# Optimization experiments

Hardware: AMD Instinct MI355X
Metric: run time of the kernel (lower is better)

Reference implementation:

```python
import jax, jax.numpy as jnp
import numpy as np

N_NODES = 50000
N_EDGES = 800000
D = 128
H = 8
DH = D // H  # 16


def setup_inputs() -> dict:
    key = jax.random.key(0)
    ks = jax.random.split(key, 9)
    x = jax.random.normal(ks[0], (N_NODES, D), dtype=jnp.float32)
    # guarantee every node has >=1 incoming edge (avoids z == 0)
    dst_rand = jax.random.randint(ks[1], (N_EDGES - N_NODES,), 0, N_NODES, dtype=jnp.int64 if jax.config.jax_enable_x64 else jnp.int32)
    dst = jnp.concatenate([jnp.arange(N_NODES, dtype=dst_rand.dtype), dst_rand])
    src = jax.random.randint(ks[2], (N_EDGES,), 0, N_NODES, dtype=dst.dtype)
    scale = 0.05
    Wq = jax.random.normal(ks[3], (D, D), dtype=jnp.float32) * scale
    Wk = jax.random.normal(ks[4], (D, D), dtype=jnp.float32) * scale
    Wv = jax.random.normal(ks[5], (D, D), dtype=jnp.float32) * scale
    bq = jax.random.normal(ks[6], (D,), dtype=jnp.float32) * scale
    bk = jax.random.normal(ks[7], (D,), dtype=jnp.float32) * scale
    bv = jax.random.normal(ks[8], (D,), dtype=jnp.float32) * scale
    return {"x": x, "src": src, "dst": dst, "Wq": Wq, "bq": bq, "Wk": Wk, "bk": bk, "Wv": Wv, "bv": bv}


def reference(x, src, dst, Wq, bq, Wk, bk, Wv, bv):
    N = x.shape[0]
    # node projections -> [N, H, DH]
    Q = (x @ Wq + bq).reshape(N, H, DH)
    K = (x @ Wk + bk).reshape(N, H, DH)
    V = (x @ Wv + bv).reshape(N, H, DH)
    scale_const = jnp.sqrt(jnp.float32(DH))
    # per-edge score: (K[src] . Q[dst]) per head, then exp-clamp  -> [E, H]
    score = jnp.einsum('ehd,ehd->eh', K[src], Q[dst])
    score = jnp.exp(jnp.clip(score / scale_const, -5.0, 5.0))
    # scatter-sum by destination node
    wV = jax.ops.segment_sum(score[:, :, None] * V[src], dst, num_segments=N)  # [N,H,DH]
    z = jax.ops.segment_sum(score, dst, num_segments=N)  # [N,H]
    attn = (wV / z[:, :, None]).reshape(N, H * DH)
    # dropout p=0 -> identity; residual
    return x + attn
```

## Files before the change

### kernel.cpp

```cpp
#include <hip/hip_runtime.h>
#include <hip/hip_bf16.h>

#define N_NODES 50000
#define N_EDGES 800000
#define D 128
#define H 8
#define DH 16
#define SCAN_CHUNK 256
#define NCHUNK ((N_NODES + SCAN_CHUNK - 1) / SCAN_CHUNK)

typedef __attribute__((ext_vector_type(8))) short short8;
typedef __attribute__((ext_vector_type(4))) float floatx4;

__device__ __forceinline__ float bfbits2f(unsigned short u) {
    union { unsigned int i; float f; } c; c.i = ((unsigned int)u) << 16; return c.f;
}
__device__ __forceinline__ short f2bfbits(float f) {
    __hip_bfloat16 h = __float2bfloat16(f);
    return *reinterpret_cast<short*>(&h);
}

__global__ __launch_bounds__(256) void prep_w_kernel(
    const float* __restrict__ Wq, const float* __restrict__ Wk,
    const float* __restrict__ Wv, __hip_bfloat16* __restrict__ Wt,
    int* __restrict__ counts)
{
    const int i = blockIdx.x * 256 + threadIdx.x;
    if (i < N_NODES) counts[i] = 0;
    if (i >= 3 * D * D) return;
    const int p = i >> 14;
    const int r = i & (D * D - 1);
    const int col = r >> 7;
    const int k = r & (D - 1);
    const float* W = (p == 0) ? Wq : (p == 1) ? Wk : Wv;
    Wt[i] = __float2bfloat16(W[k * D + col]);
}

__global__ __launch_bounds__(256) void proj_mfma_kernel(
    const float* __restrict__ x,
    const __hip_bfloat16* __restrict__ Wt,
    const float* __restrict__ bq, const float* __restrict__ bk,
    const float* __restrict__ bv,
    __hip_bfloat16* __restrict__ Qb,
    __hip_bfloat16* __restrict__ KVi)
{
    const int p    = blockIdx.y;
    const int m0   = blockIdx.x * 32;
    const int lane = threadIdx.x & 63;
    const int wv   = threadIdx.x >> 6;
    const int cb   = wv * 32;

    const short* Wp = (const short*)(Wt + p * D * D);

    floatx4 acc[2][2];
    #pragma unroll
    for (int a = 0; a < 2; ++a)
        #pragma unroll
        for (int b = 0; b < 2; ++b)
            acc[a][b] = (floatx4){0.f, 0.f, 0.f, 0.f};

    const int lr = lane & 15;
    const int lk = (lane >> 4) * 8;

    #pragma unroll
    for (int ks = 0; ks < 4; ++ks) {
        const int k0 = ks * 32 + lk;
        short8 afr[2];
        #pragma unroll
        for (int rt = 0; rt < 2; ++rt) {
            int node = m0 + rt * 16 + lr;
            if (node > N_NODES - 1) node = N_NODES - 1;
            const float4 f0 = *(const float4*)(x + node * D + k0);
            const float4 f1 = *(const float4*)(x + node * D + k0 + 4);
            afr[rt][0] = f2bfbits(f0.x); afr[rt][1] = f2bfbits(f0.y);
            afr[rt][2] = f2bfbits(f0.z); afr[rt][3] = f2bfbits(f0.w);
            afr[rt][4] = f2bfbits(f1.x); afr[rt][5] = f2bfbits(f1.y);
            afr[rt][6] = f2bfbits(f1.z); afr[rt][7] = f2bfbits(f1.w);
        }
        #pragma unroll
        for (int ct = 0; ct < 2; ++ct) {
            const int col = cb + ct * 16 + lr;
            const short8 bfr = *(const short8*)(Wp + col * D + k0);
            acc[0][ct] = __builtin_amdgcn_mfma_f32_16x16x32_bf16(afr[0], bfr, acc[0][ct], 0, 0, 0);
            acc[1][ct] = __builtin_amdgcn_mfma_f32_16x16x32_bf16(afr[1], bfr, acc[1][ct], 0, 0, 0);
        }
    }

    const float* bias = (p == 0) ? bq : (p == 1) ? bk : bv;
    #pragma unroll
    for (int rt = 0; rt < 2; ++rt) {
        #pragma unroll
        for (int ct = 0; ct < 2; ++ct) {
            const int col = cb + ct * 16 + lr;
            const float bsv = bias[col];
            #pragma unroll
            for (int r = 0; r < 4; ++r) {
                const int node = m0 + rt * 16 + (lane >> 4) * 4 + r;
                if (node < N_NODES) {
                    const float val = acc[rt][ct][r] + bsv;
                    if (p == 0)      Qb [node * D + col]              = __float2bfloat16(val);
                    else if (p == 1) KVi[node * 2 * D + 2 * col]      = __float2bfloat16(val);
                    else             KVi[node * 2 * D + 2 * col + 1]  = __float2bfloat16(val);
                }
            }
        }
    }
}

__global__ __launch_bounds__(256) void hist_kernel(
    const int* __restrict__ dst, int* __restrict__ counts)
{
    const int i = blockIdx.x * blockDim.x + threadIdx.x;
    const int stride = gridDim.x * blockDim.x;
    for (int e = i; e < N_EDGES; e += stride)
        atomicAdd(&counts[dst[e]], 1);
}

__global__ __launch_bounds__(SCAN_CHUNK) void scan_a_kernel(
    const int* __restrict__ counts, int* __restrict__ row_ptr,
    int* __restrict__ blksums)
{
    __shared__ int sd[SCAN_CHUNK];
    const int tid = threadIdx.x;
    const int i   = blockIdx.x * SCAN_CHUNK + tid;
    const int v   = (i < N_NODES) ? counts[i] : 0;
    sd[tid] = v;
    __syncthreads();
    #pragma unroll
    for (int off = 1; off < SCAN_CHUNK; off <<= 1) {
        int t = (tid >= off) ? sd[tid - off] : 0;
        __syncthreads();
        sd[tid] += t;
        __syncthreads();
    }
    if (i < N_NODES) row_ptr[i] = sd[tid] - v;
    if (tid == 0) blksums[blockIdx.x] = sd[SCAN_CHUNK - 1];
}

__global__ __launch_bounds__(SCAN_CHUNK) void scan_b_kernel(int* __restrict__ blksums)
{
    __shared__ int sd[SCAN_CHUNK];
    const int tid = threadIdx.x;
    const int v = (tid < NCHUNK) ? blksums[tid] : 0;
    sd[tid] = v;
    __syncthreads();
    #pragma unroll
    for (int off = 1; off < SCAN_CHUNK; off <<= 1) {
        int t = (tid >= off) ? sd[tid - off] : 0;
        __syncthreads();
        sd[tid] += t;
        __syncthreads();
    }
    if (tid < NCHUNK) blksums[tid] = sd[tid] - v;
}

__global__ __launch_bounds__(256) void scan_c_kernel(
    int* __restrict__ row_ptr, const int* __restrict__ blksums,
    int* __restrict__ cursor)
{
    const int i = blockIdx.x * blockDim.x + threadIdx.x;
    if (i < N_NODES) {
        const int rp = row_ptr[i] + blksums[i >> 8];
        row_ptr[i] = rp;
        cursor[i] = rp;
    }
    if (i == 0) row_ptr[N_NODES] = N_EDGES;
}

__global__ __launch_bounds__(256) void scatter_kernel(
    const int* __restrict__ dst, const int* __restrict__ src,
    int* __restrict__ cursor, int* __restrict__ srcs)
{
    const int i = blockIdx.x * blockDim.x + threadIdx.x;
    const int stride = gridDim.x * blockDim.x;
    for (int e = i; e < N_EDGES; e += stride) {
        const int pos = atomicAdd(&cursor[dst[e]], 1);
        srcs[pos] = src[e];
    }
}

__global__ __launch_bounds__(256) void aggregate_kernel(
    const int* __restrict__ row_ptr, const int* __restrict__ srcs,
    const __hip_bfloat16* __restrict__ Qb, const __hip_bfloat16* __restrict__ KVi,
    const float* __restrict__ x, float* __restrict__ out)
{
    const int lane = threadIdx.x & 63;
    const int t    = (blockIdx.x * blockDim.x + threadIdx.x) >> 6;
    if (t >= N_NODES) return;

    const unsigned int qbits = *(const unsigned int*)((const short*)Qb + t * D + 2 * lane);
    const float q0 = bfbits2f((unsigned short)(qbits & 0xffff));
    const float q1 = bfbits2f((unsigned short)(qbits >> 16));

    int i = row_ptr[t];
    const int rp1 = row_ptr[t + 1];

    float accx = 0.f, accy = 0.f, zh = 0.f;
    const short* KVs = (const short*)KVi;

    for (; i + 4 <= rp1; i += 4) {
        const int s0 = srcs[i + 0];
        const int s1 = srcs[i + 1];
        const int s2 = srcs[i + 2];
        const int s3 = srcs[i + 3];
        const ushort4 kv0 = *(const ushort4*)(KVs + (size_t)s0 * 256 + 4 * lane);
        const ushort4 kv1 = *(const ushort4*)(KVs + (size_t)s1 * 256 + 4 * lane);
        const ushort4 kv2 = *(const ushort4*)(KVs + (size_t)s2 * 256 + 4 * lane);
        const ushort4 kv3 = *(const ushort4*)(KVs + (size_t)s3 * 256 + 4 * lane);

        float p0 = bfbits2f(kv0.x) * q0 + bfbits2f(kv0.z) * q1;
        float p1 = bfbits2f(kv1.x) * q0 + bfbits2f(kv1.z) * q1;
        float p2 = bfbits2f(kv2.x) * q0 + bfbits2f(kv2.z) * q1;
        float p3 = bfbits2f(kv3.x) * q0 + bfbits2f(kv3.z) * q1;

        p0 += __shfl_xor(p0, 1); p1 += __shfl_xor(p1, 1);
        p2 += __shfl_xor(p2, 1); p3 += __shfl_xor(p3, 1);
        p0 += __shfl_xor(p0, 2); p1 += __shfl_xor(p1, 2);
        p2 += __shfl_xor(p2, 2); p3 += __shfl_xor(p3, 2);
        p0 += __shfl_xor(p0, 4); p1 += __shfl_xor(p1, 4);
        p2 += __shfl_xor(p2, 4); p3 += __shfl_xor(p3, 4);

        const float w0 = __expf(fminf(fmaxf(p0 * 0.25f, -5.0f), 5.0f));
        const float w1 = __expf(fminf(fmaxf(p1 * 0.25f, -5.0f), 5.0f));
        const float w2 = __expf(fminf(fmaxf(p2 * 0.25f, -5.0f), 5.0f));
        const float w3 = __expf(fminf(fmaxf(p3 * 0.25f, -5.0f), 5.0f));

        accx += w0 * bfbits2f(kv0.y) + w1 * bfbits2f(kv1.y)
              + w2 * bfbits2f(kv2.y) + w3 * bfbits2f(kv3.y);
        accy += w0 * bfbits2f(kv0.w) + w1 * bfbits2f(kv1.w)
              + w2 * bfbits2f(kv2.w) + w3 * bfbits2f(kv3.w);
        zh   += (w0 + w1) + (w2 + w3);
    }
    for (; i < rp1; ++i) {
        const int s = srcs[i];
        const ushort4 kv = *(const ushort4*)(KVs + (size_t)s * 256 + 4 * lane);
        float p = bfbits2f(kv.x) * q0 + bfbits2f(kv.z) * q1;
        p += __shfl_xor(p, 1);
        p += __shfl_xor(p, 2);
        p += __shfl_xor(p, 4);
        const float w = __expf(fminf(fmaxf(p * 0.25f, -5.0f), 5.0f));
        accx += w * bfbits2f(kv.y);
        accy += w * bfbits2f(kv.w);
        zh   += w;
    }

    const float inv = 1.0f / zh;
    const int base = t * D + 2 * lane;
    out[base + 0] = x[base + 0] + accx * inv;
    out[base + 1] = x[base + 1] + accy * inv;
}

extern "C" void kernel_launch(void* const* d_in, const int* in_sizes, int n_in,
                              void* d_out, int out_size, void* d_ws, size_t ws_size,
                              hipStream_t stream) {
    const float* x   = (const float*)d_in[0];
    const int*   src = (const int*)d_in[1];
    const int*   dst = (const int*)d_in[2];
    const float* Wq  = (const float*)d_in[3];
    const float* bq  = (const float*)d_in[4];
    const float* Wk  = (const float*)d_in[5];
    const float* bk  = (const float*)d_in[6];
    const float* Wv  = (const float*)d_in[7];
    const float* bv  = (const float*)d_in[8];

    __hip_bfloat16* Qb  = (__hip_bfloat16*)d_ws;
    __hip_bfloat16* KVi = Qb + (size_t)N_NODES * D;
    __hip_bfloat16* Wt  = KVi + (size_t)N_NODES * 2 * D;
    int* counts   = (int*)(Wt + 3 * D * D);
    int* row_ptr  = counts + 50048;
    int* cursor   = row_ptr + 50048;
    int* blksums  = cursor + 50048;
    int* srcs     = blksums + 256;

    float* out = (float*)d_out;

    prep_w_kernel<<<196, 256, 0, stream>>>(Wq, Wk, Wv, Wt, counts);

    proj_mfma_kernel<<<dim3((N_NODES + 31) / 32, 3), 256, 0, stream>>>(
        x, Wt, bq, bk, bv, Qb, KVi);

    hist_kernel<<<1024, 256, 0, stream>>>(dst, counts);
    scan_a_kernel<<<NCHUNK, SCAN_CHUNK, 0, stream>>>(counts, row_ptr, blksums);
    scan_b_kernel<<<1, SCAN_CHUNK, 0, stream>>>(blksums);
    scan_c_kernel<<<(N_NODES + 255) / 256, 256, 0, stream>>>(row_ptr, blksums, cursor);
    scatter_kernel<<<1024, 256, 0, stream>>>(dst, src, cursor, srcs);

    aggregate_kernel<<<(N_NODES * 64 + 255) / 256, 256, 0, stream>>>(
        row_ptr, srcs, Qb, KVi, x, out);
}
```

Before: 316.1 us.

## Fuse Q/K/V projections into one kernel with LDS-staged x and packed K/V stores

Replaces the three-way grid over Q, K and V with a single launch. Each block converts a 64-row tile of x to bf16 once into shared memory and computes all three projections from it. K and V are written as packed 32-bit pairs and Q as a transposed, column-major array with vectorised stores. The aim is to cut repeated global reads of x and the narrow 2-byte strided stores. In exchange, the aggregate kernel now reads Q with strided, uncoalesced loads, and the larger accumulator array raises register pressure.

New measurement: 276.5 us. 1.14x faster.

```diff
diff --git a/kernel.cpp b/kernel.cpp
--- a/kernel.cpp
+++ b/kernel.cpp
@@ -15,9 +15,9 @@
 __device__ __forceinline__ float bfbits2f(unsigned short u) {
     union { unsigned int i; float f; } c; c.i = ((unsigned int)u) << 16; return c.f;
 }
-__device__ __forceinline__ short f2bfbits(float f) {
+__device__ __forceinline__ unsigned short f2bfbits(float f) {
     __hip_bfloat16 h = __float2bfloat16(f);
-    return *reinterpret_cast<short*>(&h);
+    return *reinterpret_cast<unsigned short*>(&h);
 }
 
 __global__ __launch_bounds__(256) void prep_w_kernel(
@@ -41,66 +41,93 @@
     const __hip_bfloat16* __restrict__ Wt,
     const float* __restrict__ bq, const float* __restrict__ bk,
     const float* __restrict__ bv,
-    __hip_bfloat16* __restrict__ Qb,
-    __hip_bfloat16* __restrict__ KVi)
-{
-    const int p    = blockIdx.y;
-    const int m0   = blockIdx.x * 32;
-    const int lane = threadIdx.x & 63;
-    const int wv   = threadIdx.x >> 6;
+    unsigned short* __restrict__ Qt,
+    unsigned int* __restrict__ KVi)
+{
+    const int m0   = blockIdx.x * 64;
+    const int tid  = threadIdx.x;
+    const int lane = tid & 63;
+    const int wv   = tid >> 6;
     const int cb   = wv * 32;
-
-    const short* Wp = (const short*)(Wt + p * D * D);
-
-    floatx4 acc[2][2];
-    #pragma unroll
-    for (int a = 0; a < 2; ++a)
-        #pragma unroll
-        for (int b = 0; b < 2; ++b)
-            acc[a][b] = (floatx4){0.f, 0.f, 0.f, 0.f};
-
-    const int lr = lane & 15;
-    const int lk = (lane >> 4) * 8;
+    const int lr   = lane & 15;
+    const int hi   = lane >> 4;
+
+    __shared__ short xs[64][136];
+
+    {
+        const int row = tid >> 2;
+        const int c0  = (tid & 3) * 32;
+        int n = m0 + row; if (n >= N_NODES) n = N_NODES - 1;
+        const float* xr = x + (size_t)n * D + c0;
+        #pragma unroll
+        for (int i = 0; i < 8; ++i) {
+            const float4 f = *(const float4*)(xr + i * 4);
+            short4 s;
+            s.x = (short)f2bfbits(f.x); s.y = (short)f2bfbits(f.y);
+            s.z = (short)f2bfbits(f.z); s.w = (short)f2bfbits(f.w);
+            *(short4*)(&xs[row][c0 + i * 4]) = s;
+        }
+    }
+    __syncthreads();
+
+    floatx4 acc[3][4][2];
+    #pragma unroll
+    for (int p = 0; p < 3; ++p)
+        #pragma unroll
+        for (int rt = 0; rt < 4; ++rt)
+            #pragma unroll
+            for (int ct = 0; ct < 2; ++ct)
+                acc[p][rt][ct] = (floatx4){0.f, 0.f, 0.f, 0.f};
+
+    const short* Wts = (const short*)Wt;
 
     #pragma unroll
     for (int ks = 0; ks < 4; ++ks) {
-        const int k0 = ks * 32 + lk;
-        short8 afr[2];
-        #pragma unroll
-        for (int rt = 0; rt < 2; ++rt) {
-            int node = m0 + rt * 16 + lr;
-            if (node > N_NODES - 1) node = N_NODES - 1;
-            const float4 f0 = *(const float4*)(x + node * D + k0);
-            const float4 f1 = *(const float4*)(x + node * D + k0 + 4);
-            afr[rt][0] = f2bfbits(f0.x); afr[rt][1] = f2bfbits(f0.y);
-            afr[rt][2] = f2bfbits(f0.z); afr[rt][3] = f2bfbits(f0.w);
-            afr[rt][4] = f2bfbits(f1.x); afr[rt][5] = f2bfbits(f1.y);
-            afr[rt][6] = f2bfbits(f1.z); afr[rt][7] = f2bfbits(f1.w);
-        }
-        #pragma unroll
-        for (int ct = 0; ct < 2; ++ct) {
-            const int col = cb + ct * 16 + lr;
-            const short8 bfr = *(const short8*)(Wp + col * D + k0);
-            acc[0][ct] = __builtin_amdgcn_mfma_f32_16x16x32_bf16(afr[0], bfr, acc[0][ct], 0, 0, 0);
-            acc[1][ct] = __builtin_amdgcn_mfma_f32_16x16x32_bf16(afr[1], bfr, acc[1][ct], 0, 0, 0);
-        }
-    }
-
-    const float* bias = (p == 0) ? bq : (p == 1) ? bk : bv;
-    #pragma unroll
-    for (int rt = 0; rt < 2; ++rt) {
-        #pragma unroll
-        for (int ct = 0; ct < 2; ++ct) {
-            const int col = cb + ct * 16 + lr;
-            const float bsv = bias[col];
+        const int k0 = ks * 32 + hi * 8;
+
+        short8 bfr[3][2];
+        #pragma unroll
+        for (int p = 0; p < 3; ++p)
             #pragma unroll
-            for (int r = 0; r < 4; ++r) {
-                const int node = m0 + rt * 16 + (lane >> 4) * 4 + r;
-                if (node < N_NODES) {
-                    const float val = acc[rt][ct][r] + bsv;
-                    if (p == 0)      Qb [node * D + col]              = __float2bfloat16(val);
-                    else if (p == 1) KVi[node * 2 * D + 2 * col]      = __float2bfloat16(val);
-                    else             KVi[node * 2 * D + 2 * col + 1]  = __float2bfloat16(val);
+            for (int ct = 0; ct < 2; ++ct) {
+                const int col = cb + ct * 16 + lr;
+                bfr[p][ct] = *(const short8*)(Wts + ((size_t)(p * D + col) * D + k0));
+            }
+
+        short8 afr[4];
+        #pragma unroll
+        for (int rt = 0; rt < 4; ++rt)
+            afr[rt] = *(const short8*)(&xs[rt * 16 + lr][k0]);
+
+        #pragma unroll
+        for (int p = 0; p < 3; ++p)
+            #pragma unroll
+            for (int ct = 0; ct < 2; ++ct)
+                #pragma unroll
+                for (int rt = 0; rt < 4; ++rt)
+                    acc[p][rt][ct] = __builtin_amdgcn_mfma_f32_16x16x32_bf16(
+                        afr[rt], bfr[p][ct], acc[p][rt][ct], 0, 0, 0);
+    }
+
+    #pragma unroll
+    for (int ct = 0; ct < 2; ++ct) {
+        const int col = cb + ct * 16 + lr;
+        const float bqv = bq[col], bkv = bk[col], bvv = bv[col];
+        #pragma unroll
+        for (int rt = 0; rt < 4; ++rt) {
+            const int node0 = m0 + rt * 16 + hi * 4;
+            if (node0 < N_NODES) {
+                ushort4 qs;
+                qs.x = f2bfbits(acc[0][rt][ct][0] + bqv);
+                qs.y = f2bfbits(acc[0][rt][ct][1] + bqv);
+                qs.z = f2bfbits(acc[0][rt][ct][2] + bqv);
+                qs.w = f2bfbits(acc[0][rt][ct][3] + bqv);
+                *(ushort4*)(Qt + (size_t)col * N_NODES + node0) = qs;
+                #pragma unroll
+                for (int r = 0; r < 4; ++r) {
+                    const unsigned int kk = f2bfbits(acc[1][rt][ct][r] + bkv);
+                    const unsigned int vv = f2bfbits(acc[2][rt][ct][r] + bvv);
+                    KVi[(size_t)(node0 + r) * 128 + col] = kk | (vv << 16);
                 }
             }
         }
@@ -181,37 +208,36 @@
 
 __global__ __launch_bounds__(256) void aggregate_kernel(
     const int* __restrict__ row_ptr, const int* __restrict__ srcs,
-    const __hip_bfloat16* __restrict__ Qb, const __hip_bfloat16* __restrict__ KVi,
+    const unsigned short* __restrict__ Qt, const unsigned int* __restrict__ KVi,
     const float* __restrict__ x, float* __restrict__ out)
 {
     const int lane = threadIdx.x & 63;
     const int t    = (blockIdx.x * blockDim.x + threadIdx.x) >> 6;
     if (t >= N_NODES) return;
 
-    const unsigned int qbits = *(const unsigned int*)((const short*)Qb + t * D + 2 * lane);
-    const float q0 = bfbits2f((unsigned short)(qbits & 0xffff));
-    const float q1 = bfbits2f((unsigned short)(qbits >> 16));
+    const float q0 = bfbits2f(Qt[(size_t)(2 * lane)     * N_NODES + t]);
+    const float q1 = bfbits2f(Qt[(size_t)(2 * lane + 1) * N_NODES + t]);
 
     int i = row_ptr[t];
     const int rp1 = row_ptr[t + 1];
 
     float accx = 0.f, accy = 0.f, zh = 0.f;
-    const short* KVs = (const short*)KVi;
+    const unsigned long long* KVs = (const unsigned long long*)KVi;
 
     for (; i + 4 <= rp1; i += 4) {
         const int s0 = srcs[i + 0];
         const int s1 = srcs[i + 1];
         const int s2 = srcs[i + 2];
         const int s3 = srcs[i + 3];
-        const ushort4 kv0 = *(const ushort4*)(KVs + (size_t)s0 * 256 + 4 * lane);
-        const ushort4 kv1 = *(const ushort4*)(KVs + (size_t)s1 * 256 + 4 * lane);
-        const ushort4 kv2 = *(const ushort4*)(KVs + (size_t)s2 * 256 + 4 * lane);
-        const ushort4 kv3 = *(const ushort4*)(KVs + (size_t)s3 * 256 + 4 * lane);
-
-        float p0 = bfbits2f(kv0.x) * q0 + bfbits2f(kv0.z) * q1;
-        float p1 = bfbits2f(kv1.x) * q0 + bfbits2f(kv1.z) * q1;
-        float p2 = bfbits2f(kv2.x) * q0 + bfbits2f(kv2.z) * q1;
-        float p3 = bfbits2f(kv3.x) * q0 + bfbits2f(kv3.z) * q1;
+        const unsigned long long kv0 = KVs[(size_t)s0 * 64 + lane];
+        const unsigned long long kv1 = KVs[(size_t)s1 * 64 + lane];
+        const unsigned long long kv2 = KVs[(size_t)s2 * 64 + lane];
+        const unsigned long long kv3 = KVs[(size_t)s3 * 64 + lane];
+
+        float p0 = bfbits2f((unsigned short)kv0) * q0 + bfbits2f((unsigned short)(kv0 >> 32)) * q1;
+        float p1 = bfbits2f((unsigned short)kv1) * q0 + bfbits2f((unsigned short)(kv1 >> 32)) * q1;
+        float p2 = bfbits2f((unsigned short)kv2) * q0 + bfbits2f((unsigned short)(kv2 >> 32)) * q1;
+        float p3 = bfbits2f((unsigned short)kv3) * q0 + bfbits2f((unsigned short)(kv3 >> 32)) * q1;
 
         p0 += __shfl_xor(p0, 1); p1 += __shfl_xor(p1, 1);
         p2 += __shfl_xor(p2, 1); p3 += __shfl_xor(p3, 1);
@@ -225,22 +251,22 @@
         const float w2 = __expf(fminf(fmaxf(p2 * 0.25f, -5.0f), 5.0f));
         const float w3 = __expf(fminf(fmaxf(p3 * 0.25f, -5.0f), 5.0f));
 
-        accx += w0 * bfbits2f(kv0.y) + w1 * bfbits2f(kv1.y)
-              + w2 * bfbits2f(kv2.y) + w3 * bfbits2f(kv3.y);
-        accy += w0 * bfbits2f(kv0.w) + w1 * bfbits2f(kv1.w)
-              + w2 * bfbits2f(kv2.w) + w3 * bfbits2f(kv3.w);
+        accx += w0 * bfbits2f((unsigned short)(kv0 >> 16)) + w1 * bfbits2f((unsigned short)(kv1 >> 16))
+              + w2 * bfbits2f((unsigned short)(kv2 >> 16)) + w3 * bfbits2f((unsigned short)(kv3 >> 16));
+        accy += w0 * bfbits2f((unsigned short)(kv0 >> 48)) + w1 * bfbits2f((unsigned short)(kv1 >> 48))
+              + w2 * bfbits2f((unsigned short)(kv2 >> 48)) + w3 * bfbits2f((unsigned short)(kv3 >> 48));
         zh   += (w0 + w1) + (w2 + w3);
     }
     for (; i < rp1; ++i) {
         const int s = srcs[i];
-        const ushort4 kv = *(const ushort4*)(KVs + (size_t)s * 256 + 4 * lane);
-        float p = bfbits2f(kv.x) * q0 + bfbits2f(kv.z) * q1;
+        const unsigned long long kv = KVs[(size_t)s * 64 + lane];
+        float p = bfbits2f((unsigned short)kv) * q0 + bfbits2f((unsigned short)(kv >> 32)) * q1;
         p += __shfl_xor(p, 1);
         p += __shfl_xor(p, 2);
         p += __shfl_xor(p, 4);
         const float w = __expf(fminf(fmaxf(p * 0.25f, -5.0f), 5.0f));
-        accx += w * bfbits2f(kv.y);
-        accy += w * bfbits2f(kv.w);
+        accx += w * bfbits2f((unsigned short)(kv >> 16));
+        accy += w * bfbits2f((unsigned short)(kv >> 48));
         zh   += w;
     }
 
@@ -263,9 +289,9 @@
     const float* Wv  = (const float*)d_in[7];
     const float* bv  = (const float*)d_in[8];
 
-    __hip_bfloat16* Qb  = (__hip_bfloat16*)d_ws;
-    __hip_bfloat16* KVi = Qb + (size_t)N_NODES * D;
-    __hip_bfloat16* Wt  = KVi + (size_t)N_NODES * 2 * D;
+    unsigned short* Qt  = (unsigned short*)d_ws;
+    unsigned int*   KVi = (unsigned int*)(Qt + (size_t)D * N_NODES);
+    __hip_bfloat16* Wt  = (__hip_bfloat16*)(KVi + (size_t)N_NODES * 128);
     int* counts   = (int*)(Wt + 3 * D * D);
     int* row_ptr  = counts + 50048;
     int* cursor   = row_ptr + 50048;
@@ -276,8 +302,8 @@
 
     prep_w_kernel<<<196, 256, 0, stream>>>(Wq, Wk, Wv, Wt, counts);
 
-    proj_mfma_kernel<<<dim3((N_NODES + 31) / 32, 3), 256, 0, stream>>>(
-        x, Wt, bq, bk, bv, Qb, KVi);
+    proj_mfma_kernel<<<(N_NODES + 63) / 64, 256, 0, stream>>>(
+        x, Wt, bq, bk, bv, Qt, KVi);
 
     hist_kernel<<<1024, 256, 0, stream>>>(dst, counts);
     scan_a_kernel<<<NCHUNK, SCAN_CHUNK, 0, stream>>>(counts, row_ptr, blksums);
@@ -286,5 +312,5 @@
     scatter_kernel<<<1024, 256, 0, stream>>>(dst, src, cursor, srcs);
 
     aggregate_kernel<<<(N_NODES * 64 + 255) / 256, 256, 0, stream>>>(
-        row_ptr, srcs, Qb, KVi, x, out);
-}
+        row_ptr, srcs, Qt, KVi, x, out);
+}
```
